# Kernel optimization log

Measured on AMD Instinct MI355X. Metric: run time of the kernel, lower is better.

Reference implementation:

```python
import jax, jax.numpy as jnp
import numpy as np

PS = 4        # bkg_patch_size
PD = 1        # replicate pad
UFSTRIDE = 2  # patch-extraction stride
STRIDE = 1    # correlation stride
SCALE = 10.0  # softmax_scale


def pad_edge(x):
    return jnp.pad(x, ((0, 0), (0, 0), (PD, PD), (PD, PD)), mode='edge')


def unfold(x, ps, stride):
    # x: (B,C,H,W) -> (B, L, C, ps, ps), row-major over patch grid (matches F.unfold)
    B, C, H, W = x.shape
    oh = (H - ps) // stride + 1
    ow = (W - ps) // stride + 1
    ih = jnp.arange(oh)[:, None] * stride + jnp.arange(ps)[None, :]  # (oh, ps)
    iw = jnp.arange(ow)[:, None] * stride + jnp.arange(ps)[None, :]  # (ow, ps)
    p = x[:, :, ih][:, :, :, :, iw]            # (B,C,oh,ps,ow,ps)
    p = p.transpose(0, 2, 4, 1, 3, 5)          # (B,oh,ow,C,ps,ps)
    return p.reshape(B, oh * ow, C, ps, ps)


def diag3(x):
    # conv2d with 3x3 identity kernel, padding=1: out[i,j] = in[i-1,j-1]+in[i,j]+in[i+1,j+1]
    B, one, N, M = x.shape
    xp = jnp.pad(x, ((0, 0), (0, 0), (1, 1), (1, 1)))
    return xp[:, :, 0:N, 0:M] + xp[:, :, 1:N + 1, 1:M + 1] + xp[:, :, 2:N + 2, 2:M + 2]


def setup_inputs() -> dict:
    key = jax.random.key(0)
    k1, k2, k3 = jax.random.split(key, 3)
    B, C, H, W = 4, 64, 64, 64
    f = jax.random.normal(k1, (B, C, H, W), dtype=jnp.float32)
    b = jax.random.normal(k2, (B, C, H, W), dtype=jnp.float32)
    mask = (jax.random.uniform(k3, (B, 1, H, W)) < 0.25).astype(jnp.float32)
    return {"f": f, "b": b, "mask": mask}


def reference(f, b, mask):
    B, C, H, W = b.shape
    maskc = 1.0 - mask
    # --- get_conv_kernel: per-(batch,channel) L2-normalize b, extract patch kernels ---
    bn = b / jnp.sqrt(jnp.sum(b * b, axis=(2, 3), keepdims=True) + 1e-8)
    kernel = unfold(pad_edge(bn), PS, UFSTRIDE)                 # (B, L, C, ps, ps)
    mk = unfold(pad_edge(maskc), PS, UFSTRIDE)                  # (B, L, 1, ps, ps)
    mmk = jnp.mean(mk, axis=(2, 3, 4))[:, :, None, None]        # (B, L, 1, 1)
    L = kernel.shape[1]

    # --- batched grouped cross-correlation: conv f with per-sample patch kernels ---
    fpatch = unfold(pad_edge(f), PS, STRIDE)                    # (B, P, C, ps, ps)
    hs = (H + 2 * PD - PS) // STRIDE + 1
    ws = (W + 2 * PD - PS) // STRIDE + 1
    cos = jnp.einsum('bpcij,blcij->blp', fpatch, kernel)        # (B, L, P)
    cos = cos.reshape(B, L, hs, ws)

    # --- fuse: diagonal 3x3 convs along two axis pairings ---
    hb, wb = H // 2, W // 2
    cs = L
    c1 = diag3(cos.reshape(B, 1, cs, hs * ws))
    c1 = c1.reshape(B, 1, hb, wb, hs, ws).transpose(0, 1, 3, 2, 5, 4).reshape(B, 1, cs, hs * ws)
    c1 = diag3(c1)
    c1 = c1.reshape(B, 1, hb, wb, hs, ws).transpose(0, 1, 3, 2, 5, 4)
    cos = c1.reshape(B, cs, hs, ws)

    # --- irregular mask logic ---
    mp = unfold(pad_edge(maskc), PS, STRIDE)                    # (B, P, 1, ps, ps)
    mmp = jnp.mean(mp, axis=(2, 3, 4)).reshape(B, 1, hs, ws)    # (B, 1, hs, ws)
    mm = (mmk > mmp).astype(cos.dtype)                          # (B, L, hs, ws)
    ppp = (mmp > 0.5).astype(cos.dtype)
    mm = mm * ppp + (mmk == 1.0).astype(cos.dtype)
    mm = (mm > 0).astype(cos.dtype)

    cos = cos * mm
    return jax.nn.softmax(cos * SCALE, axis=1)
```

## Files before the change

kernel.cpp:

```cpp
#include <hip/hip_runtime.h>
#include <math.h>

#define NB 4
#define NC 64
#define NL 1024
#define NP 3969
#define PHW 63

typedef unsigned short ushort_t;
typedef __attribute__((ext_vector_type(8))) short short8;
typedef __attribute__((ext_vector_type(16))) float floatx16;

#define A_BSTRIDE 1048576
#define B_BSTRIDE 4128768

__global__ __launch_bounds__(256) void norm_kernel(const float* __restrict__ bsrc,
                                                   float* __restrict__ invn) {
    int bc = blockIdx.x;
    const float* src = bsrc + (size_t)bc * 4096;
    float s = 0.f;
    for (int i = threadIdx.x; i < 4096; i += 256) { float v = src[i]; s += v * v; }
#pragma unroll
    for (int off = 32; off > 0; off >>= 1) s += __shfl_down(s, off, 64);
    __shared__ float part[4];
    if ((threadIdx.x & 63) == 0) part[threadIdx.x >> 6] = s;
    __syncthreads();
    if (threadIdx.x == 0) {
        float t = part[0] + part[1] + part[2] + part[3];
        invn[bc] = 1.0f / sqrtf(t + 1e-8f);
    }
}

__global__ __launch_bounds__(256) void stats_kernel(const float* __restrict__ mask,
                                                    float* __restrict__ mmk,
                                                    float* __restrict__ mmp) {
    int id = blockIdx.x * 256 + threadIdx.x;
    if (id < NB * NL) {
        int b = id >> 10, l = id & 1023;
        int lh = l >> 5, lw = l & 31;
        const float* m = mask + b * 4096;
        float s = 0.f;
#pragma unroll
        for (int i = 0; i < 4; ++i) {
            int r = min(max(2 * lh - 1 + i, 0), 63);
#pragma unroll
            for (int j = 0; j < 4; ++j) {
                int c = min(max(2 * lw - 1 + j, 0), 63);
                s += 1.0f - m[r * 64 + c];
            }
        }
        mmk[id] = s * (1.0f / 16.0f);
    } else {
        int id2 = id - NB * NL;
        if (id2 < NB * NP) {
            int b = id2 / NP, p = id2 - b * NP;
            int ph = p / PHW, pw = p - ph * PHW;
            const float* m = mask + b * 4096;
            float s = 0.f;
#pragma unroll
            for (int i = 0; i < 4; ++i) {
                int r = min(max(ph - 1 + i, 0), 63);
#pragma unroll
                for (int j = 0; j < 4; ++j) {
                    int c = min(max(pw - 1 + j, 0), 63);
                    s += 1.0f - m[r * 64 + c];
                }
            }
            mmp[id2] = s * (1.0f / 16.0f);
        }
    }
}

__device__ inline void split_bf16(float v, ushort_t& hv, ushort_t& lv) {
    unsigned u = __float_as_uint(v);
    unsigned rr = u + 0x7FFFu + ((u >> 16) & 1u);
    hv = (ushort_t)(rr >> 16);
    float fh = __uint_as_float(((unsigned)hv) << 16);
    float remv = v - fh;
    unsigned u2 = __float_as_uint(remv);
    unsigned rr2 = u2 + 0x7FFFu + ((u2 >> 16) & 1u);
    lv = (ushort_t)(rr2 >> 16);
}

__device__ inline int frag_addr(int row, int kc) {
    return ((row >> 5) * 64 + kc) * 512 + (row & 31) * 8;
}

__global__ __launch_bounds__(256) void splitA_kernel(const float* __restrict__ bsrc,
                                                     const float* __restrict__ invn,
                                                     ushort_t* __restrict__ Ahi,
                                                     ushort_t* __restrict__ Alo) {
    __shared__ float fl[32 * 257];
    int lh = blockIdx.x, b = blockIdx.y, chalf = blockIdx.z;
    int t = threadIdx.x;
#pragma unroll
    for (int q = 0; q < 32; ++q) {
        int idx = t + (q << 8);
        int cl = idx >> 8, rem = idx & 255;
        int i = rem >> 6, s = rem & 63;
        int c = (chalf << 5) + cl;
        int r = min(max(2 * lh - 1 + i, 0), 63);
        fl[cl * 257 + rem] = bsrc[(((size_t)((b << 6) + c)) << 12) + (r << 6) + s];
    }
    __syncthreads();
    ushort_t* Ah = Ahi + (size_t)b * A_BSTRIDE;
    ushort_t* Al = Alo + (size_t)b * A_BSTRIDE;
#pragma unroll
    for (int q = 0; q < 4; ++q) {
        int pair = t + (q << 8);
        int lw = pair & 31, cl = pair >> 5;
        int c = (chalf << 5) + cl;
        float scale = invn[(b << 6) + c];
        const float* row = fl + cl * 257;
        __align__(16) ushort_t h[16];
        __align__(16) ushort_t lo[16];
#pragma unroll
        for (int i = 0; i < 4; ++i)
#pragma unroll
            for (int j = 0; j < 4; ++j) {
                int s = min(max(2 * lw - 1 + j, 0), 63);
                split_bf16(row[i * 64 + s] * scale, h[i * 4 + j], lo[i * 4 + j]);
            }
        int a = (lh * 64 + c) * 512 + lw * 8;
        *(uint4*)(Ah + a)       = *(uint4*)h;
        *(uint4*)(Ah + a + 256) = *(uint4*)(h + 8);
        *(uint4*)(Al + a)       = *(uint4*)lo;
        *(uint4*)(Al + a + 256) = *(uint4*)(lo + 8);
    }
}

__global__ __launch_bounds__(256) void splitB_kernel(const float* __restrict__ fsrc,
                                                     ushort_t* __restrict__ Bhi,
                                                     ushort_t* __restrict__ Blo) {
    __shared__ float fl[32 * 257];
    int ph = blockIdx.x, b = blockIdx.y, chalf = blockIdx.z;
    int t = threadIdx.x;
#pragma unroll
    for (int q = 0; q < 32; ++q) {
        int idx = t + (q << 8);
        int cl = idx >> 8, rem = idx & 255;
        int i = rem >> 6, s = rem & 63;
        int c = (chalf << 5) + cl;
        int r = min(max(ph - 1 + i, 0), 63);
        fl[cl * 257 + rem] = fsrc[(((size_t)((b << 6) + c)) << 12) + (r << 6) + s];
    }
    __syncthreads();
    ushort_t* Bh = Bhi + (size_t)b * B_BSTRIDE;
    ushort_t* Bl = Blo + (size_t)b * B_BSTRIDE;
#pragma unroll
    for (int q = 0; q < 8; ++q) {
        int pair = t + (q << 8);
        int pw = pair & 63, cl = pair >> 6;
        if (pw < PHW) {
            int c = (chalf << 5) + cl;
            const float* row = fl + cl * 257;
            __align__(16) ushort_t h[16];
            __align__(16) ushort_t lo[16];
#pragma unroll
            for (int i = 0; i < 4; ++i)
#pragma unroll
                for (int j = 0; j < 4; ++j) {
                    int s = min(max(pw - 1 + j, 0), 63);
                    split_bf16(row[i * 64 + s], h[i * 4 + j], lo[i * 4 + j]);
                }
            int p = ph * PHW + pw;
            int a = frag_addr(p, c);
            *(uint4*)(Bh + a)       = *(uint4*)h;
            *(uint4*)(Bh + a + 256) = *(uint4*)(h + 8);
            *(uint4*)(Bl + a)       = *(uint4*)lo;
            *(uint4*)(Bl + a + 256) = *(uint4*)(lo + 8);
        }
    }
    if (ph == 62) {
        uint4 z = {0, 0, 0, 0};
#pragma unroll
        for (int q = 0; q < 4; ++q) {
            int idx = t + (q << 8);
            int r31 = idx & 31, cl = idx >> 5;
            int c = (chalf << 5) + cl;
            if (r31 < 31) {
                int a = (124 * 64 + c) * 512 + (1 + r31) * 8;
                *(uint4*)(Bh + a) = z; *(uint4*)(Bh + a + 256) = z;
                *(uint4*)(Bl + a) = z; *(uint4*)(Bl + a + 256) = z;
            }
            int a2 = (125 * 64 + c) * 512 + r31 * 8;
            *(uint4*)(Bh + a2) = z; *(uint4*)(Bh + a2 + 256) = z;
            *(uint4*)(Bl + a2) = z; *(uint4*)(Bl + a2 + 256) = z;
        }
    }
}

__global__ __launch_bounds__(256) void gemm_kernel(
    const ushort_t* __restrict__ Ahi, const ushort_t* __restrict__ Alo,
    const ushort_t* __restrict__ Bhi, const ushort_t* __restrict__ Blo,
    float* __restrict__ Rt) {
    int tid = threadIdx.x;
    int lane = tid & 63, w = tid >> 6;
    int bx = blockIdx.x;
    int b = blockIdx.y;
    int ltile = ((bx & 3) << 2) + w;
    int ptile = bx >> 2;
    int l0 = ltile << 6, p0 = ptile << 6;

    size_t la = (size_t)b * A_BSTRIDE + ((l0 >> 5) * 64) * 512 + lane * 8;
    size_t lb = (size_t)b * B_BSTRIDE + ((p0 >> 5) * 64) * 512 + lane * 8;
    const ushort_t* ah0 = Ahi + la;  const ushort_t* ah1 = ah0 + 32768;
    const ushort_t* al0 = Alo + la;  const ushort_t* al1 = al0 + 32768;
    const ushort_t* bh0 = Bhi + lb;  const ushort_t* bh1 = bh0 + 32768;
    const ushort_t* bl0 = Blo + lb;  const ushort_t* bl1 = bl0 + 32768;

    floatx16 acc[2][2];
#pragma unroll
    for (int i = 0; i < 2; ++i)
#pragma unroll
        for (int j = 0; j < 2; ++j)
#pragma unroll
            for (int r = 0; r < 16; ++r) acc[i][j][r] = 0.f;

    short8 fa[8], fb[8];

#define LOADC(dst, kc)                                   \
    do {                                                 \
        int o = (kc) * 512;                              \
        dst[0] = *(const short8*)(ah0 + o);              \
        dst[1] = *(const short8*)(ah1 + o);              \
        dst[2] = *(const short8*)(al0 + o);              \
        dst[3] = *(const short8*)(al1 + o);              \
        dst[4] = *(const short8*)(bh0 + o);              \
        dst[5] = *(const short8*)(bh1 + o);              \
        dst[6] = *(const short8*)(bl0 + o);              \
        dst[7] = *(const short8*)(bl1 + o);              \
    } while (0)

#define COMP(f)                                                                                       \
    do {                                                                                              \
        _Pragma("unroll")                                                                             \
        for (int pt = 0; pt < 2; ++pt)                                                                \
            _Pragma("unroll")                                                                         \
            for (int lt = 0; lt < 2; ++lt) {                                                          \
                acc[pt][lt] = __builtin_amdgcn_mfma_f32_32x32x16_bf16(f[4 + pt], f[0 + lt], acc[pt][lt], 0, 0, 0); \
                acc[pt][lt] = __builtin_amdgcn_mfma_f32_32x32x16_bf16(f[4 + pt], f[2 + lt], acc[pt][lt], 0, 0, 0); \
                acc[pt][lt] = __builtin_amdgcn_mfma_f32_32x32x16_bf16(f[6 + pt], f[0 + lt], acc[pt][lt], 0, 0, 0); \
            }                                                                                         \
    } while (0)

    LOADC(fa, 0);
    for (int kc = 0; kc < 64; kc += 2) {
        LOADC(fb, kc + 1);
        COMP(fa);
        if (kc + 2 < 64) LOADC(fa, kc + 2);
        COMP(fb);
    }
#undef LOADC
#undef COMP

    int x = lane & 31, kg = lane >> 5;
#pragma unroll
    for (int pt = 0; pt < 2; ++pt)
#pragma unroll
        for (int lt = 0; lt < 2; ++lt)
#pragma unroll
            for (int r = 0; r < 16; ++r) {
                int p = p0 + (pt << 5) + (r & 3) + ((r >> 2) << 3) + (kg << 2);
                int l = l0 + (lt << 5) + x;
                if (p < NP) Rt[((size_t)b * NP + p) * NL + l] = acc[pt][lt][r];
            }
}

__global__ __launch_bounds__(256) void diag1_kernel(const float* __restrict__ Rt,
                                                    float* __restrict__ D1) {
    int p = blockIdx.x, b = blockIdx.y;
    int t = threadIdx.x;
    const float* base = Rt + ((size_t)b * NP + p) * NL;
    int l4 = t << 2;
    float4 r = *(const float4*)(base + l4);
    if (p > 0) {
        const float* pm = base - NL;
        r.x += (l4 > 0) ? pm[l4 - 1] : 0.f;
        r.y += pm[l4];
        r.z += pm[l4 + 1];
        r.w += pm[l4 + 2];
    }
    if (p < NP - 1) {
        const float* pp = base + NL;
        r.x += pp[l4 + 1];
        r.y += pp[l4 + 2];
        r.z += pp[l4 + 3];
        r.w += (l4 + 4 < NL) ? pp[l4 + 4] : 0.f;
    }
    *(float4*)(D1 + ((size_t)b * NP + p) * NL + l4) = r;
}

__global__ __launch_bounds__(256) void softmax_rows_kernel(const float* __restrict__ D1,
                                                           const float* __restrict__ mmkA,
                                                           const float* __restrict__ mmpA,
                                                           float* __restrict__ E) {
    __shared__ float red[8];
    int p = blockIdx.x, b = blockIdx.y;
    int ph = p / PHW, pw = p - ph * PHW;
    int t = threadIdx.x;
    int lane = t & 63, w = t >> 6;
    int l0 = t << 2;

    const float* Db = D1 + (size_t)b * NP * NL;
    const float* rowc = Db + (size_t)p * NL;
    bool okm = (p != 0), okp = (p != 3968);
    int Pm = (ph > 0) ? p - 63 : 3905 + pw;
    int Pp = (ph < 62) ? p + 63 : pw + 1;
    const float* rowm = Db + (size_t)(okm ? Pm : 0) * NL;
    const float* rowp = Db + (size_t)(okp ? Pp : 0) * NL;

    float4 vc = *(const float4*)(rowc + l0);
    float4 vm = {0.f, 0.f, 0.f, 0.f}, vp = {0.f, 0.f, 0.f, 0.f};
    if (okm) {
        if (l0 >= 32) vm = *(const float4*)(rowm + l0 - 32);
        else {
            vm.x = (l0 == 0) ? 0.f : rowm[l0 + 991];
            vm.y = rowm[l0 + 992];
            vm.z = rowm[l0 + 993];
            vm.w = rowm[l0 + 994];
        }
    }
    if (okp) {
        if (l0 < 992) vp = *(const float4*)(rowp + l0 + 32);
        else {
            vp.x = rowp[l0 - 991];
            vp.y = rowp[l0 - 990];
            vp.z = rowp[l0 - 989];
            vp.w = (l0 + 3 == 1023) ? 0.f : rowp[l0 - 988];
        }
    }
    float mmpv = mmpA[b * NP + p];
    float4 km = *(const float4*)(mmkA + b * NL + l0);
    float lg[4];
    float fsum[4] = {vc.x + vm.x + vp.x, vc.y + vm.y + vp.y,
                     vc.z + vm.z + vp.z, vc.w + vm.w + vp.w};
    float kk[4] = {km.x, km.y, km.z, km.w};
#pragma unroll
    for (int i = 0; i < 4; ++i) {
        float mmv = (((kk[i] > mmpv) && (mmpv > 0.5f)) || (kk[i] == 1.0f)) ? 1.0f : 0.0f;
        lg[i] = fsum[i] * mmv * 10.0f;
    }
    float mx = fmaxf(fmaxf(lg[0], lg[1]), fmaxf(lg[2], lg[3]));
#pragma unroll
    for (int off = 32; off >= 1; off >>= 1) mx = fmaxf(mx, __shfl_xor(mx, off, 64));
    if (lane == 0) red[w] = mx;
    __syncthreads();
    mx = fmaxf(fmaxf(red[0], red[1]), fmaxf(red[2], red[3]));
    float e[4];
    float s = 0.f;
#pragma unroll
    for (int i = 0; i < 4; ++i) { e[i] = expf(lg[i] - mx); s += e[i]; }
#pragma unroll
    for (int off = 32; off >= 1; off >>= 1) s += __shfl_xor(s, off, 64);
    if (lane == 0) red[4 + w] = s;
    __syncthreads();
    float rinv = 1.0f / (red[4] + red[5] + red[6] + red[7]);
    float4 ev = {e[0] * rinv, e[1] * rinv, e[2] * rinv, e[3] * rinv};
    *(float4*)(E + (((size_t)b * NP + p) << 10) + l0) = ev;
}

__global__ __launch_bounds__(256) void transpose_kernel(const float* __restrict__ E,
                                                        float* __restrict__ out) {
    __shared__ float tile[63 * 65];
    int pt = blockIdx.x;
    int lt = blockIdx.y;
    int b  = blockIdx.z;
    int t = threadIdx.x;
    int p0 = pt * 63, l0 = lt << 6;
    const float* Eb = E + ((size_t)b * NP << 10);
    {
        int j = t & 63, i4 = t >> 6;
#pragma unroll
        for (int k = 0; k < 16; ++k) {
            int i = (k << 2) + i4;
            if (i < 63) tile[i * 65 + j] = Eb[((size_t)(p0 + i) << 10) + l0 + j];
        }
    }
    __syncthreads();
    {
        int ii = t & 63, jj4 = t >> 6;
        if (ii < 63) {
#pragma unroll
            for (int k = 0; k < 16; ++k) {
                int jj = (k << 2) + jj4;
                out[((size_t)b * NL + l0 + jj) * NP + p0 + ii] = tile[ii * 65 + jj];
            }
        }
    }
}

extern "C" void kernel_launch(void* const* d_in, const int* in_sizes, int n_in,
                              void* d_out, int out_size, void* d_ws, size_t ws_size,
                              hipStream_t stream) {
    const float* f    = (const float*)d_in[0];
    const float* b    = (const float*)d_in[1];
    const float* mask = (const float*)d_in[2];
    float* out = (float*)d_out;

    float* Rt = (float*)d_out;

    float* wsf = (float*)d_ws;
    float* D1 = wsf;
    float* E  = wsf + 16257024;
    ushort_t* Ahi = (ushort_t*)d_ws;
    ushort_t* Alo = Ahi + (size_t)NB * A_BSTRIDE;
    ushort_t* Bhi = Alo + (size_t)NB * A_BSTRIDE;
    ushort_t* Blo = Bhi + (size_t)NB * B_BSTRIDE;
    float* invn = wsf + 32514048;
    float* mmk = invn + 256;
    float* mmp = mmk + 4096;

    norm_kernel<<<dim3(256), dim3(256), 0, stream>>>(b, invn);
    stats_kernel<<<dim3(79), dim3(256), 0, stream>>>(mask, mmk, mmp);
    splitA_kernel<<<dim3(32, 4, 2), dim3(256), 0, stream>>>(b, invn, Ahi, Alo);
    splitB_kernel<<<dim3(63, 4, 2), dim3(256), 0, stream>>>(f, Bhi, Blo);
    gemm_kernel<<<dim3(252, 4), dim3(256), 0, stream>>>(Ahi, Alo, Bhi, Blo, Rt);
    diag1_kernel<<<dim3(3969, 4), dim3(256), 0, stream>>>(Rt, D1);
    softmax_rows_kernel<<<dim3(3969, 4), dim3(256), 0, stream>>>(D1, mmk, mmp, E);
    transpose_kernel<<<dim3(63, 16, 4), dim3(256), 0, stream>>>(E, out);
}
```

Baseline: 302.6 us.

## Fuse first diagonal pass into softmax kernel and deepen GEMM load pipeline

Removes the separate diag1 kernel and its D1 intermediate. The softmax kernel now rebuilds the three needed diagonal-summed rows (current, previous, next) straight from the GEMM output into shared memory. This saves a full write and read of a 16M-float buffer and one launch, at the cost of reading about three times as many Rt rows per block. The GEMM also moves from a double-buffered to a 4-deep register prefetch, with clamped chunk indices and launch_bounds(256,2), to better hide global-load latency. The deeper pipeline raises register pressure.

New measurement: 297.9 us. No clear change (-1.5%).

```diff
diff --git a/kernel.cpp b/kernel.cpp
--- a/kernel.cpp
+++ b/kernel.cpp
@@ -190,7 +190,7 @@
     }
 }
 
-__global__ __launch_bounds__(256) void gemm_kernel(
+__global__ __launch_bounds__(256, 2) void gemm_kernel(
     const ushort_t* __restrict__ Ahi, const ushort_t* __restrict__ Alo,
     const ushort_t* __restrict__ Bhi, const ushort_t* __restrict__ Blo,
     float* __restrict__ Rt) {
@@ -217,7 +217,7 @@
 #pragma unroll
             for (int r = 0; r < 16; ++r) acc[i][j][r] = 0.f;
 
-    short8 fa[8], fb[8];
+    short8 f[4][8];
 
 #define LOADC(dst, kc)                                   \
     do {                                                 \
@@ -232,24 +232,30 @@
         dst[7] = *(const short8*)(bl1 + o);              \
     } while (0)
 
-#define COMP(f)                                                                                       \
+#define COMP(g)                                                                                       \
     do {                                                                                              \
         _Pragma("unroll")                                                                             \
         for (int pt = 0; pt < 2; ++pt)                                                                \
             _Pragma("unroll")                                                                         \
             for (int lt = 0; lt < 2; ++lt) {                                                          \
-                acc[pt][lt] = __builtin_amdgcn_mfma_f32_32x32x16_bf16(f[4 + pt], f[0 + lt], acc[pt][lt], 0, 0, 0); \
-                acc[pt][lt] = __builtin_amdgcn_mfma_f32_32x32x16_bf16(f[4 + pt], f[2 + lt], acc[pt][lt], 0, 0, 0); \
-                acc[pt][lt] = __builtin_amdgcn_mfma_f32_32x32x16_bf16(f[6 + pt], f[0 + lt], acc[pt][lt], 0, 0, 0); \
+                acc[pt][lt] = __builtin_amdgcn_mfma_f32_32x32x16_bf16(g[4 + pt], g[0 + lt], acc[pt][lt], 0, 0, 0); \
+                acc[pt][lt] = __builtin_amdgcn_mfma_f32_32x32x16_bf16(g[4 + pt], g[2 + lt], acc[pt][lt], 0, 0, 0); \
+                acc[pt][lt] = __builtin_amdgcn_mfma_f32_32x32x16_bf16(g[6 + pt], g[0 + lt], acc[pt][lt], 0, 0, 0); \
             }                                                                                         \
     } while (0)
 
-    LOADC(fa, 0);
-    for (int kc = 0; kc < 64; kc += 2) {
-        LOADC(fb, kc + 1);
-        COMP(fa);
-        if (kc + 2 < 64) LOADC(fa, kc + 2);
-        COMP(fb);
+    LOADC(f[0], 0);
+    LOADC(f[1], 1);
+    LOADC(f[2], 2);
+    for (int kc = 0; kc < 64; kc += 4) {
+        LOADC(f[3], min(kc + 3, 63));
+        COMP(f[0]);
+        LOADC(f[0], min(kc + 4, 63));
+        COMP(f[1]);
+        LOADC(f[1], min(kc + 5, 63));
+        COMP(f[2]);
+        LOADC(f[2], min(kc + 6, 63));
+        COMP(f[3]);
     }
 #undef LOADC
 #undef COMP
@@ -267,34 +273,11 @@
             }
 }
 
-__global__ __launch_bounds__(256) void diag1_kernel(const float* __restrict__ Rt,
-                                                    float* __restrict__ D1) {
-    int p = blockIdx.x, b = blockIdx.y;
-    int t = threadIdx.x;
-    const float* base = Rt + ((size_t)b * NP + p) * NL;
-    int l4 = t << 2;
-    float4 r = *(const float4*)(base + l4);
-    if (p > 0) {
-        const float* pm = base - NL;
-        r.x += (l4 > 0) ? pm[l4 - 1] : 0.f;
-        r.y += pm[l4];
-        r.z += pm[l4 + 1];
-        r.w += pm[l4 + 2];
-    }
-    if (p < NP - 1) {
-        const float* pp = base + NL;
-        r.x += pp[l4 + 1];
-        r.y += pp[l4 + 2];
-        r.z += pp[l4 + 3];
-        r.w += (l4 + 4 < NL) ? pp[l4 + 4] : 0.f;
-    }
-    *(float4*)(D1 + ((size_t)b * NP + p) * NL + l4) = r;
-}
-
-__global__ __launch_bounds__(256) void softmax_rows_kernel(const float* __restrict__ D1,
-                                                           const float* __restrict__ mmkA,
-                                                           const float* __restrict__ mmpA,
-                                                           float* __restrict__ E) {
+__global__ __launch_bounds__(256) void softmax_fused_kernel(const float* __restrict__ Rt,
+                                                            const float* __restrict__ mmkA,
+                                                            const float* __restrict__ mmpA,
+                                                            float* __restrict__ E) {
+    __shared__ float ld0[1024], ld1[1024], ld2[1024];
     __shared__ float red[8];
     int p = blockIdx.x, b = blockIdx.y;
     int ph = p / PHW, pw = p - ph * PHW;
@@ -302,32 +285,52 @@
     int lane = t & 63, w = t >> 6;
     int l0 = t << 2;
 
-    const float* Db = D1 + (size_t)b * NP * NL;
-    const float* rowc = Db + (size_t)p * NL;
     bool okm = (p != 0), okp = (p != 3968);
     int Pm = (ph > 0) ? p - 63 : 3905 + pw;
     int Pp = (ph < 62) ? p + 63 : pw + 1;
-    const float* rowm = Db + (size_t)(okm ? Pm : 0) * NL;
-    const float* rowp = Db + (size_t)(okp ? Pp : 0) * NL;
-
-    float4 vc = *(const float4*)(rowc + l0);
+
+    const float* Rb = Rt + (size_t)b * NP * NL;
+#define BUILD(dst, q)                                                   \
+    do {                                                                \
+        const float* base = Rb + (size_t)(q) * NL;                      \
+        float4 r = *(const float4*)(base + l0);                         \
+        if ((q) > 0) {                                                  \
+            const float* pm = base - NL;                                \
+            r.x += (l0 > 0) ? pm[l0 - 1] : 0.f;                         \
+            r.y += pm[l0];  r.z += pm[l0 + 1];  r.w += pm[l0 + 2];      \
+        }                                                               \
+        if ((q) < NP - 1) {                                             \
+            const float* pp = base + NL;                                \
+            r.x += pp[l0 + 1];  r.y += pp[l0 + 2];  r.z += pp[l0 + 3];  \
+            r.w += (l0 + 4 < NL) ? pp[l0 + 4] : 0.f;                    \
+        }                                                               \
+        *(float4*)(dst + l0) = r;                                       \
+    } while (0)
+
+    BUILD(ld0, p);
+    if (okm) BUILD(ld1, Pm);
+    if (okp) BUILD(ld2, Pp);
+#undef BUILD
+    __syncthreads();
+
+    float4 vc = *(const float4*)(ld0 + l0);
     float4 vm = {0.f, 0.f, 0.f, 0.f}, vp = {0.f, 0.f, 0.f, 0.f};
     if (okm) {
-        if (l0 >= 32) vm = *(const float4*)(rowm + l0 - 32);
+        if (l0 >= 32) vm = *(const float4*)(ld1 + l0 - 32);
         else {
-            vm.x = (l0 == 0) ? 0.f : rowm[l0 + 991];
-            vm.y = rowm[l0 + 992];
-            vm.z = rowm[l0 + 993];
-            vm.w = rowm[l0 + 994];
+            vm.x = (l0 == 0) ? 0.f : ld1[l0 + 991];
+            vm.y = ld1[l0 + 992];
+            vm.z = ld1[l0 + 993];
+            vm.w = ld1[l0 + 994];
         }
     }
     if (okp) {
-        if (l0 < 992) vp = *(const float4*)(rowp + l0 + 32);
+        if (l0 < 992) vp = *(const float4*)(ld2 + l0 + 32);
         else {
-            vp.x = rowp[l0 - 991];
-            vp.y = rowp[l0 - 990];
-            vp.z = rowp[l0 - 989];
-            vp.w = (l0 + 3 == 1023) ? 0.f : rowp[l0 - 988];
+            vp.x = ld2[l0 - 991];
+            vp.y = ld2[l0 - 990];
+            vp.z = ld2[l0 - 989];
+            vp.w = (l0 + 3 == 1023) ? 0.f : ld2[l0 - 988];
         }
     }
     float mmpv = mmpA[b * NP + p];
@@ -401,7 +404,6 @@
     float* Rt = (float*)d_out;
 
     float* wsf = (float*)d_ws;
-    float* D1 = wsf;
     float* E  = wsf + 16257024;
     ushort_t* Ahi = (ushort_t*)d_ws;
     ushort_t* Alo = Ahi + (size_t)NB * A_BSTRIDE;
@@ -416,7 +418,6 @@
     splitA_kernel<<<dim3(32, 4, 2), dim3(256), 0, stream>>>(b, invn, Ahi, Alo);
     splitB_kernel<<<dim3(63, 4, 2), dim3(256), 0, stream>>>(f, Bhi, Blo);
     gemm_kernel<<<dim3(252, 4), dim3(256), 0, stream>>>(Ahi, Alo, Bhi, Blo, Rt);
-    diag1_kernel<<<dim3(3969, 4), dim3(256), 0, stream>>>(Rt, D1);
-    softmax_rows_kernel<<<dim3(3969, 4), dim3(256), 0, stream>>>(D1, mmk, mmp, E);
+    softmax_fused_kernel<<<dim3(3969, 4), dim3(256), 0, stream>>>(Rt, mmk, mmp, E);
     transpose_kernel<<<dim3(63, 16, 4), dim3(256), 0, stream>>>(E, out);
 }
```
